# Kernel optimization log

Hardware: AMD Instinct MI355X
Metric: run time of the kernel (lower is better)

## Reference

```python
import jax, jax.numpy as jnp
import numpy as np

BATCH = 1_000_000
NUM_BINS = 37  # num_classes == 37 -> ranges [0, 13, 26, 37]
STARTS = jnp.array([0, 13, 26], dtype=jnp.int32)
ENDS = jnp.array([13, 26, 37], dtype=jnp.int32)
NEG_INF = jnp.float32(-1e30)
LOG_CLAMP = -100.0  # torch BCE clamps log terms at -100


def setup_inputs() -> dict:
    key = jax.random.key(0)
    k1, k2, k3 = jax.random.split(key, 3)
    preds = jax.random.normal(k1, (BATCH, NUM_BINS), dtype=jnp.float32)
    labels = jax.random.normal(k2, (BATCH, NUM_BINS), dtype=jnp.float32)
    obj_classes = jax.random.randint(k3, (BATCH,), 0, 3, dtype=jnp.int32)
    weights = jnp.ones((3,), dtype=jnp.float32)
    return {"preds": preds, "labels": labels, "weights": weights,
            "obj_classes": obj_classes}


def reference(preds, labels, weights, obj_classes):
    # Per-sample ragged slice [start, end) expressed as a mask over the 37 bins.
    idx = jnp.arange(NUM_BINS)
    s = STARTS[obj_classes][:, None]  # (B, 1)
    e = ENDS[obj_classes][:, None]    # (B, 1)
    mask = (idx >= s) & (idx < e)     # (B, 37)

    # Softmax restricted to the active slice (masked positions -> -inf logits).
    logp = jax.nn.log_softmax(jnp.where(mask, preds, NEG_INF), axis=-1)
    p = jnp.exp(logp)
    t = jax.nn.softmax(jnp.where(mask, labels, NEG_INF), axis=-1)

    # BCE(p, t) summed over the slice (size_average=False):
    # -(t*log p + (1-t)*log(1-p)), with torch-style log clamping at -100.
    logp_c = jnp.maximum(logp, LOG_CLAMP)
    log1mp = jnp.maximum(jnp.log1p(-p), LOG_CLAMP)
    bce = jnp.where(mask, -(t * logp_c + (1.0 - t) * log1mp), 0.0)

    per_sample = bce.sum(axis=-1) * weights[obj_classes]  # (B,)
    losses = jax.ops.segment_sum(per_sample, obj_classes, num_segments=3)
    total = losses.sum() / jnp.float32(preds.shape[0])
    return (total[None], losses[0][None], losses[1][None], losses[2][None])
```

## Files before the change

### kernel.cpp

```cpp
#include <hip/hip_runtime.h>

constexpr int BATCH  = 1000000;
constexpr int NBINS  = 37;
constexpr int TPB    = 256;
constexpr int WPB    = 4;
constexpr int ROWS   = 64;
constexpr int TDW    = ROWS * NBINS;
constexpr int NV     = 9;
constexpr int REMDW  = NV * 64 * 4;
constexpr int NBLK   = 512;
constexpr int NWAVES = NBLK * WPB;
constexpr int NTILES = BATCH / ROWS;
constexpr float NEG_BIG  = -1e30f;
constexpr float LOGCLAMP = -100.0f;

__global__ __launch_bounds__(TPB, 2)
void adviser_loss_kernel(const float* __restrict__ preds,
                         const float* __restrict__ labels,
                         const float* __restrict__ weights,
                         const int* __restrict__ obj,
                         float* __restrict__ out)
{
    __shared__ float lds[WPB][2][TDW];
    __shared__ float cls_sum[3];

    const int tid  = threadIdx.x;
    const int lane = tid & 63;
    const int w    = tid >> 6;
    const int gw   = blockIdx.x * WPB + w;

    if (tid < 3) cls_sum[tid] = 0.0f;
    __syncthreads();

    const float w0 = weights[0], w1 = weights[1], w2 = weights[2];

    float* myP = &lds[w][0][0];
    float* myT = &lds[w][1][0];

    float4 Pv[NV], Lv[NV];
    float  Pf = 0.0f, Lf = 0.0f;
    int    creg = 0;

    auto prefetch = [&](int t) {
        const float4* gp = (const float4*)(preds  + (size_t)t * TDW);
        const float4* gl = (const float4*)(labels + (size_t)t * TDW);
        #pragma unroll
        for (int k = 0; k < NV; ++k) {
            Pv[k] = gp[lane + k * 64];
            Lv[k] = gl[lane + k * 64];
        }
        Pf = ((const float*)gp)[REMDW + lane];
        Lf = ((const float*)gl)[REMDW + lane];
        creg = obj[t * ROWS + lane];
    };

    float a0 = 0.0f, a1 = 0.0f, a2 = 0.0f;

    prefetch(gw);
    for (int t = gw; t < NTILES; t += NWAVES) {
        #pragma unroll
        for (int k = 0; k < NV; ++k) {
            ((float4*)myP)[lane + k * 64] = Pv[k];
            ((float4*)myT)[lane + k * 64] = Lv[k];
        }
        myP[REMDW + lane] = Pf;
        myT[REMDW + lane] = Lf;
        const int c = creg;

        const int nt = t + NWAVES;
        if (nt < NTILES) prefetch(nt);
        __builtin_amdgcn_sched_barrier(0);

        const float wt = (c == 0) ? w0 : ((c == 1) ? w1 : w2);
        const int   s  = 13 * c;
        const int   L  = (c == 2) ? 11 : 13;
        const int   base = lane * NBINS + s;

        float pv[13], ep[13], et[13];
        float Z = 0.0f, Zt = 0.0f;
        #pragma unroll
        for (int j = 0; j < 13; ++j) {
            const float x = (j < L) ? myP[base + j] : NEG_BIG;
            const float y = (j < L) ? myT[base + j] : NEG_BIG;
            pv[j] = x;
            ep[j] = __expf(x);  Z  += ep[j];
            et[j] = __expf(y);  Zt += et[j];
        }
        const float logZ  = __logf(Z);
        const float rcpZ  = __builtin_amdgcn_rcpf(Z);
        const float rcpZt = __builtin_amdgcn_rcpf(Zt);

        float acc = 0.0f;
        #pragma unroll
        for (int j = 0; j < 13; ++j) {
            const float logp = pv[j] - logZ;
            const float p    = ep[j] * rcpZ;
            const float ca   = fmaxf(logp, LOGCLAMP);
            const float cb   = fmaxf(__logf(fmaxf(1.0f - p, 0.0f)), LOGCLAMP);
            const float t_   = et[j] * rcpZt;
            acc += cb + t_ * (ca - cb);
        }
        const float per = (-acc) * wt;
        a0 += (c == 0) ? per : 0.0f;
        a1 += (c == 1) ? per : 0.0f;
        a2 += (c == 2) ? per : 0.0f;
    }

    #pragma unroll
    for (int off = 32; off > 0; off >>= 1) {
        a0 += __shfl_down(a0, off, 64);
        a1 += __shfl_down(a1, off, 64);
        a2 += __shfl_down(a2, off, 64);
    }
    if (lane == 0) {
        atomicAdd(&cls_sum[0], a0);
        atomicAdd(&cls_sum[1], a1);
        atomicAdd(&cls_sum[2], a2);
    }
    __syncthreads();
    if (tid == 0) {
        const float s0 = cls_sum[0], s1 = cls_sum[1], s2 = cls_sum[2];
        atomicAdd(&out[1], s0);
        atomicAdd(&out[2], s1);
        atomicAdd(&out[3], s2);
        atomicAdd(&out[0], (s0 + s1 + s2) * (1.0f / (float)BATCH));
    }
}

extern "C" void kernel_launch(void* const* d_in, const int* in_sizes, int n_in,
                              void* d_out, int out_size, void* d_ws, size_t ws_size,
                              hipStream_t stream) {
    const float* preds   = (const float*)d_in[0];
    const float* labels  = (const float*)d_in[1];
    const float* weights = (const float*)d_in[2];
    const int*   obj     = (const int*)d_in[3];
    float* out = (float*)d_out;

    hipMemsetAsync(out, 0, (size_t)out_size * sizeof(float), stream);
    adviser_loss_kernel<<<NBLK, TPB, 0, stream>>>(preds, labels, weights, obj, out);
}
```

Baseline: 349.4 us.

## Replace LDS-staged persistent tiles with one-row-per-thread direct gathers

```diff
diff --git a/kernel.cpp b/kernel.cpp
--- a/kernel.cpp
+++ b/kernel.cpp
@@ -1,118 +1,79 @@
 #include <hip/hip_runtime.h>
 
-constexpr int BATCH  = 1000000;
-constexpr int NBINS  = 37;
-constexpr int TPB    = 256;
-constexpr int WPB    = 4;
-constexpr int ROWS   = 64;
-constexpr int TDW    = ROWS * NBINS;
-constexpr int NV     = 9;
-constexpr int REMDW  = NV * 64 * 4;
-constexpr int NBLK   = 512;
-constexpr int NWAVES = NBLK * WPB;
-constexpr int NTILES = BATCH / ROWS;
+constexpr int   BATCH   = 1000000;
+constexpr int   NBINS   = 37;
+constexpr long long TOTDW = (long long)BATCH * NBINS;
+constexpr int   TPB     = 256;
+constexpr int   NBLK    = (BATCH + TPB - 1) / TPB;
 constexpr float NEG_BIG  = -1e30f;
 constexpr float LOGCLAMP = -100.0f;
 
-__global__ __launch_bounds__(TPB, 2)
+__global__ __launch_bounds__(TPB, 6)
 void adviser_loss_kernel(const float* __restrict__ preds,
                          const float* __restrict__ labels,
                          const float* __restrict__ weights,
                          const int* __restrict__ obj,
                          float* __restrict__ out)
 {
-    __shared__ float lds[WPB][2][TDW];
     __shared__ float cls_sum[3];
-
-    const int tid  = threadIdx.x;
-    const int lane = tid & 63;
-    const int w    = tid >> 6;
-    const int gw   = blockIdx.x * WPB + w;
-
+    const int tid = threadIdx.x;
     if (tid < 3) cls_sum[tid] = 0.0f;
     __syncthreads();
 
-    const float w0 = weights[0], w1 = weights[1], w2 = weights[2];
+    const int  row_raw = blockIdx.x * TPB + tid;
+    const bool valid   = row_raw < BATCH;
+    const int  row     = valid ? row_raw : BATCH - 1;
 
-    float* myP = &lds[w][0][0];
-    float* myT = &lds[w][1][0];
+    const int   c = obj[row];
+    const float w = weights[c];
+    const int   s = 13 * c;
+    const int   L = (c == 2) ? 11 : 13;
+    const long long base = (long long)row * NBINS + s;
 
-    float4 Pv[NV], Lv[NV];
-    float  Pf = 0.0f, Lf = 0.0f;
-    int    creg = 0;
-
-    auto prefetch = [&](int t) {
-        const float4* gp = (const float4*)(preds  + (size_t)t * TDW);
-        const float4* gl = (const float4*)(labels + (size_t)t * TDW);
-        #pragma unroll
-        for (int k = 0; k < NV; ++k) {
-            Pv[k] = gp[lane + k * 64];
-            Lv[k] = gl[lane + k * 64];
-        }
-        Pf = ((const float*)gp)[REMDW + lane];
-        Lf = ((const float*)gl)[REMDW + lane];
-        creg = obj[t * ROWS + lane];
-    };
-
-    float a0 = 0.0f, a1 = 0.0f, a2 = 0.0f;
-
-    prefetch(gw);
-    for (int t = gw; t < NTILES; t += NWAVES) {
-        #pragma unroll
-        for (int k = 0; k < NV; ++k) {
-            ((float4*)myP)[lane + k * 64] = Pv[k];
-            ((float4*)myT)[lane + k * 64] = Lv[k];
-        }
-        myP[REMDW + lane] = Pf;
-        myT[REMDW + lane] = Lf;
-        const int c = creg;
-
-        const int nt = t + NWAVES;
-        if (nt < NTILES) prefetch(nt);
-        __builtin_amdgcn_sched_barrier(0);
-
-        const float wt = (c == 0) ? w0 : ((c == 1) ? w1 : w2);
-        const int   s  = 13 * c;
-        const int   L  = (c == 2) ? 11 : 13;
-        const int   base = lane * NBINS + s;
-
-        float pv[13], ep[13], et[13];
-        float Z = 0.0f, Zt = 0.0f;
-        #pragma unroll
-        for (int j = 0; j < 13; ++j) {
-            const float x = (j < L) ? myP[base + j] : NEG_BIG;
-            const float y = (j < L) ? myT[base + j] : NEG_BIG;
-            pv[j] = x;
-            ep[j] = __expf(x);  Z  += ep[j];
-            et[j] = __expf(y);  Zt += et[j];
-        }
-        const float logZ  = __logf(Z);
-        const float rcpZ  = __builtin_amdgcn_rcpf(Z);
-        const float rcpZt = __builtin_amdgcn_rcpf(Zt);
-
-        float acc = 0.0f;
-        #pragma unroll
-        for (int j = 0; j < 13; ++j) {
-            const float logp = pv[j] - logZ;
-            const float p    = ep[j] * rcpZ;
-            const float ca   = fmaxf(logp, LOGCLAMP);
-            const float cb   = fmaxf(__logf(fmaxf(1.0f - p, 0.0f)), LOGCLAMP);
-            const float t_   = et[j] * rcpZt;
-            acc += cb + t_ * (ca - cb);
-        }
-        const float per = (-acc) * wt;
-        a0 += (c == 0) ? per : 0.0f;
-        a1 += (c == 1) ? per : 0.0f;
-        a2 += (c == 2) ? per : 0.0f;
+    float pv[13], lv[13];
+    #pragma unroll
+    for (int j = 0; j < 13; ++j) {
+        long long idx = base + j;
+        if (j >= 11) idx = (idx < TOTDW) ? idx : (TOTDW - 1);
+        pv[j] = preds[idx];
+        lv[j] = labels[idx];
     }
 
+    float Z = 0.0f, Zt = 0.0f;
+    #pragma unroll
+    for (int j = 0; j < 13; ++j) {
+        const bool act = (j < L);
+        pv[j] = act ? pv[j] : NEG_BIG;
+        lv[j] = act ? lv[j] : NEG_BIG;
+        Z  += __expf(pv[j]);
+        Zt += __expf(lv[j]);
+    }
+    const float logZ  = __logf(Z);
+    const float rcpZ  = __builtin_amdgcn_rcpf(Z);
+    const float rcpZt = __builtin_amdgcn_rcpf(Zt);
+
+    float acc = 0.0f;
+    #pragma unroll
+    for (int j = 0; j < 13; ++j) {
+        const float logp = pv[j] - logZ;
+        const float p    = __expf(pv[j]) * rcpZ;
+        const float ca   = fmaxf(logp, LOGCLAMP);
+        const float cb   = fmaxf(__logf(fmaxf(1.0f - p, 0.0f)), LOGCLAMP);
+        const float t    = __expf(lv[j]) * rcpZt;
+        acc += cb + t * (ca - cb);
+    }
+    const float per = valid ? (-acc) * w : 0.0f;
+
+    float a0 = (c == 0) ? per : 0.0f;
+    float a1 = (c == 1) ? per : 0.0f;
+    float a2 = (c == 2) ? per : 0.0f;
     #pragma unroll
     for (int off = 32; off > 0; off >>= 1) {
         a0 += __shfl_down(a0, off, 64);
         a1 += __shfl_down(a1, off, 64);
         a2 += __shfl_down(a2, off, 64);
     }
-    if (lane == 0) {
+    if ((tid & 63) == 0) {
         atomicAdd(&cls_sum[0], a0);
         atomicAdd(&cls_sum[1], a1);
         atomicAdd(&cls_sum[2], a2);
```

Result: slower. 420.0 us (+20.2%).
